# Kernel optimization log

Hardware: AMD Instinct MI355X
Metric: run time of the kernel (lower is better)

Reference implementation:

```python
import jax, jax.numpy as jnp
import numpy as np

N_I = 500_000   # 'indivi' nodes (dst)
N_H = 200_000   # 'house' nodes
F_I = 32        # indivi feature dim
F_H = 16        # house feature dim
EF = 8          # edge_attr dim
E1 = 2_000_000  # house->indivi edges
E2 = 2_000_000  # indivi->indivi edges


def setup_inputs() -> dict:
    key = jax.random.key(0)
    ks = jax.random.split(key, 16)
    return {
        "x_indivi": jax.random.normal(ks[0], (N_I, F_I), jnp.float32),
        "x_house": jax.random.normal(ks[1], (N_H, F_H), jnp.float32),
        "edge_attr_h2i": jax.random.normal(ks[2], (E1, EF), jnp.float32),
        "edge_attr_i2i": jax.random.normal(ks[3], (E2, EF), jnp.float32),
        "W_edge_h2i": jax.random.normal(ks[4], (F_H, EF), jnp.float32) * 0.1,
        "b_edge_h2i": jax.random.normal(ks[5], (F_H,), jnp.float32) * 0.1,
        "W_edge_i2i": jax.random.normal(ks[6], (F_I, EF), jnp.float32) * 0.1,
        "b_edge_i2i": jax.random.normal(ks[7], (F_I,), jnp.float32) * 0.1,
        "W_root_h2i": jax.random.normal(ks[8], (1, F_I), jnp.float32) * 0.1,
        "bias_h2i": jax.random.normal(ks[9], (1,), jnp.float32) * 0.1,
        "W_root_i2i": jax.random.normal(ks[10], (1, F_I), jnp.float32) * 0.1,
        "bias_i2i": jax.random.normal(ks[11], (1,), jnp.float32) * 0.1,
        "src_h2i": jax.random.randint(ks[12], (E1,), 0, N_H, jnp.int32),
        "dst_h2i": jax.random.randint(ks[13], (E1,), 0, N_I, jnp.int32),
        "src_i2i": jax.random.randint(ks[14], (E2,), 0, N_I, jnp.int32),
        "dst_i2i": jax.random.randint(ks[15], (E2,), 0, N_I, jnp.int32),
    }


def _nnconv(x_src, x_dst, edge_attr, src, dst, W_edge, b_edge, W_root, bias, num_dst):
    # Edge MLP -> per-edge weight matrix of shape [F_src, out=1], flattened to [E, F_src]
    w = edge_attr @ W_edge.T + b_edge                     # [E, F_src]
    # message_e = x_src[src_e] @ w_e  (out_channels = 1)
    msg = jnp.sum(x_src[src] * w, axis=-1, keepdims=True)  # [E, 1]
    agg = jax.ops.segment_sum(msg, dst, num_segments=num_dst)  # [N_dst, 1]
    # root transform on destination features + bias
    return agg + x_dst @ W_root.T + bias                  # [N_dst, 1]


def reference(x_indivi, x_house, edge_attr_h2i, edge_attr_i2i,
              W_edge_h2i, b_edge_h2i, W_edge_i2i, b_edge_i2i,
              W_root_h2i, bias_h2i, W_root_i2i, bias_i2i,
              src_h2i, dst_h2i, src_i2i, dst_i2i):
    out_h = _nnconv(x_house, x_indivi, edge_attr_h2i, src_h2i, dst_h2i,
                    W_edge_h2i, b_edge_h2i, W_root_h2i, bias_h2i, N_I)
    out_i = _nnconv(x_indivi, x_indivi, edge_attr_i2i, src_i2i, dst_i2i,
                    W_edge_i2i, b_edge_i2i, W_root_i2i, bias_i2i, N_I)
    # HeteroConv(aggr='sum') over the two relations targeting 'indivi'
    return out_h + out_i
```

## Files before the change

kernel.cpp:

```cpp
#include <hip/hip_runtime.h>

#define N_I 500000
#define N_H 200000
#define E1  2000000
#define E2  2000000
#define TOTAL_E (E1 + E2)

#define BSHIFT 12
#define NB 128
#define NBK ((N_I + 4095) / 4096)
#define CHUNK 2048
#define NWG ((TOTAL_E + CHUNK - 1) / CHUNK)
#define WPT 8

template<int F, bool ROOT>
__global__ __launch_bounds__(256) void precompute_g(
    const float* __restrict__ x, const float* __restrict__ W, const float* __restrict__ b,
    float* __restrict__ g, int n,
    const float* __restrict__ rW1, const float* __restrict__ rW2,
    const float* __restrict__ rb1, const float* __restrict__ rb2,
    float* __restrict__ out)
{
    __shared__ float Wf[F * 8];
    __shared__ float bv[F];
    __shared__ float wr[F];

    for (int i = threadIdx.x; i < F * 8; i += 256) Wf[i] = W[i];
    if (threadIdx.x < F) {
        bv[threadIdx.x] = b[threadIdx.x];
        if (ROOT) wr[threadIdx.x] = rW1[threadIdx.x] + rW2[threadIdx.x];
    }
    __syncthreads();

    int nid = blockIdx.x * 256 + threadIdx.x;
    if (nid >= n) return;

    float xv[F];
    const float4* xp = (const float4*)(x + (size_t)nid * F);
    #pragma unroll
    for (int q = 0; q < F / 4; q++) {
        float4 v = xp[q];
        xv[q*4+0] = v.x; xv[q*4+1] = v.y; xv[q*4+2] = v.z; xv[q*4+3] = v.w;
    }

    float acc[9];
    #pragma unroll
    for (int k = 0; k < 9; k++) acc[k] = 0.f;

    #pragma unroll
    for (int j = 0; j < F; j++) {
        float4 w0 = *(const float4*)(Wf + j * 8);
        float4 w1 = *(const float4*)(Wf + j * 8 + 4);
        float xj = xv[j];
        acc[0] = fmaf(xj, w0.x, acc[0]);
        acc[1] = fmaf(xj, w0.y, acc[1]);
        acc[2] = fmaf(xj, w0.z, acc[2]);
        acc[3] = fmaf(xj, w0.w, acc[3]);
        acc[4] = fmaf(xj, w1.x, acc[4]);
        acc[5] = fmaf(xj, w1.y, acc[5]);
        acc[6] = fmaf(xj, w1.z, acc[6]);
        acc[7] = fmaf(xj, w1.w, acc[7]);
        acc[8] = fmaf(xj, bv[j], acc[8]);
    }

    float4* gp = (float4*)(g + (size_t)nid * 12);
    gp[0] = make_float4(acc[0], acc[1], acc[2], acc[3]);
    gp[1] = make_float4(acc[4], acc[5], acc[6], acc[7]);
    gp[2] = make_float4(acc[8], 0.f, 0.f, 0.f);

    if (ROOT) {
        float r = rb1[0] + rb2[0];
        #pragma unroll
        for (int j = 0; j < F; j++) r = fmaf(xv[j], wr[j], r);
        out[nid] = r;
    }
}

__device__ __forceinline__ void edge_msg(
    int t,
    const int* __restrict__ src1, const int* __restrict__ dst1,
    const float* __restrict__ ea1, const float* __restrict__ g1,
    const int* __restrict__ src2, const int* __restrict__ dst2,
    const float* __restrict__ ea2, const float* __restrict__ g2,
    int& d_out, float& m_out)
{
    const int* srcp; const int* dstp; const float* eap; const float* gp;
    int e;
    if (t < E1) { e = t;      srcp = src1; dstp = dst1; eap = ea1; gp = g1; }
    else        { e = t - E1; srcp = src2; dstp = dst2; eap = ea2; gp = g2; }

    int s = srcp[e];
    d_out = dstp[e];
    const float4* ap = (const float4*)(eap + (size_t)e * 8);
    float4 a0 = ap[0];
    float4 a1 = ap[1];
    const float4* gr = (const float4*)(gp + (size_t)s * 12);
    float4 ga = gr[0];
    float4 gb = gr[1];
    float4 gc = gr[2];

    float msg = gc.x;
    msg = fmaf(a0.x, ga.x, msg);
    msg = fmaf(a0.y, ga.y, msg);
    msg = fmaf(a0.z, ga.z, msg);
    msg = fmaf(a0.w, ga.w, msg);
    msg = fmaf(a1.x, gb.x, msg);
    msg = fmaf(a1.y, gb.y, msg);
    msg = fmaf(a1.z, gb.z, msg);
    msg = fmaf(a1.w, gb.w, msg);
    m_out = msg;
}

__global__ __launch_bounds__(256) void msg_hist_kernel(
    const int* __restrict__ src1, const int* __restrict__ dst1,
    const float* __restrict__ ea1, const float* __restrict__ g1,
    const int* __restrict__ src2, const int* __restrict__ dst2,
    const float* __restrict__ ea2, const float* __restrict__ g2,
    float* __restrict__ msg_out, int* __restrict__ H)
{
    __shared__ int hist[NB];
    if (threadIdx.x < NB) hist[threadIdx.x] = 0;
    __syncthreads();

    int base = blockIdx.x * CHUNK;
    #pragma unroll
    for (int it = 0; it < CHUNK / 256; ++it) {
        int t = base + it * 256 + threadIdx.x;
        if (t < TOTAL_E) {
            int d; float m;
            edge_msg(t, src1, dst1, ea1, g1, src2, dst2, ea2, g2, d, m);
            msg_out[t] = m;
            atomicAdd(&hist[d >> BSHIFT], 1);
        }
    }
    __syncthreads();
    if (threadIdx.x < NB) H[blockIdx.x * NB + threadIdx.x] = hist[threadIdx.x];
}

__global__ __launch_bounds__(256) void scan_cols_kernel(int* __restrict__ H,
                                                        int* __restrict__ total)
{
    __shared__ int sums[256];
    int b = blockIdx.x;
    int tid = threadIdx.x;

    int vals[WPT];
    int s = 0;
    #pragma unroll
    for (int k = 0; k < WPT; k++) {
        int w = tid * WPT + k;
        vals[k] = (w < NWG) ? H[w * NB + b] : 0;
        s += vals[k];
    }
    sums[tid] = s;
    __syncthreads();
    for (int off = 1; off < 256; off <<= 1) {
        int t = (tid >= off) ? sums[tid - off] : 0;
        __syncthreads();
        sums[tid] += t;
        __syncthreads();
    }
    int run = sums[tid] - s;
    #pragma unroll
    for (int k = 0; k < WPT; k++) {
        int w = tid * WPT + k;
        if (w < NWG) H[w * NB + b] = run;
        run += vals[k];
    }
    if (tid == 255) total[b] = sums[255];
}

__global__ __launch_bounds__(128) void scan_base_kernel(const int* __restrict__ total,
                                                        int* __restrict__ base)
{
    __shared__ int v[NB];
    int tid = threadIdx.x;
    int orig = total[tid];
    v[tid] = orig;
    __syncthreads();
    for (int off = 1; off < NB; off <<= 1) {
        int t = (tid >= off) ? v[tid - off] : 0;
        __syncthreads();
        v[tid] += t;
        __syncthreads();
    }
    base[tid] = v[tid] - orig;
}

__global__ __launch_bounds__(256) void scatter_kernel(
    const int* __restrict__ dst1, const int* __restrict__ dst2,
    const float* __restrict__ msg, const int* __restrict__ H,
    const int* __restrict__ base, uint2* __restrict__ pairs)
{
    __shared__ int cnt[NB];
    __shared__ int sv[NB];
    __shared__ int gbase[NB];
    __shared__ unsigned short bkt[CHUNK];
    __shared__ uint2 lp[CHUNK];

    int tid = threadIdx.x;
    if (tid < NB) cnt[tid] = 0;
    __syncthreads();

    int cbase = blockIdx.x * CHUNK;
    int dloc[CHUNK / 256];
    #pragma unroll
    for (int it = 0; it < CHUNK / 256; ++it) {
        int t = cbase + it * 256 + tid;
        int d = -1;
        if (t < TOTAL_E) {
            d = (t < E1) ? dst1[t] : dst2[t - E1];
            atomicAdd(&cnt[d >> BSHIFT], 1);
        }
        dloc[it] = d;
    }
    __syncthreads();

    int myc = 0;
    if (tid < NB) { myc = cnt[tid]; sv[tid] = myc; }
    __syncthreads();
    for (int off = 1; off < NB; off <<= 1) {
        int t = (tid < NB && tid >= off) ? sv[tid - off] : 0;
        __syncthreads();
        if (tid < NB) sv[tid] += t;
        __syncthreads();
    }
    if (tid < NB) {
        int loff = sv[tid] - myc;
        gbase[tid] = H[blockIdx.x * NB + tid] + base[tid] - loff;
        cnt[tid] = loff;
    }
    __syncthreads();

    #pragma unroll
    for (int it = 0; it < CHUNK / 256; ++it) {
        int t = cbase + it * 256 + tid;
        if (t < TOTAL_E) {
            int d = dloc[it];
            float m = msg[t];
            int b = d >> BSHIFT;
            int slot = atomicAdd(&cnt[b], 1);
            lp[slot] = make_uint2((unsigned)d, __float_as_uint(m));
            bkt[slot] = (unsigned short)b;
        }
    }
    __syncthreads();

    int nvalid = TOTAL_E - cbase;
    if (nvalid > CHUNK) nvalid = CHUNK;
    for (int i = tid; i < nvalid; i += 256) {
        int b = bkt[i];
        pairs[gbase[b] + i] = lp[i];
    }
}

__global__ __launch_bounds__(512) void reduce_kernel(
    const uint2* __restrict__ pairs, const int* __restrict__ base,
    const int* __restrict__ total, float* __restrict__ part)
{
    __shared__ float acc[4096];
    for (int i = threadIdx.x; i < 4096; i += 512) acc[i] = 0.f;
    __syncthreads();

    int b = blockIdx.x >> 2;
    int k = blockIdx.x & 3;
    int start = base[b];
    int cnt = total[b];
    int q = (cnt + 3) >> 2;
    int s0 = k * q;
    int s1 = s0 + q; if (s1 > cnt) s1 = cnt;

    for (int i = s0 + threadIdx.x; i < s1; i += 512) {
        uint2 p = pairs[start + i];
        atomicAdd(&acc[p.x & 4095], __uint_as_float(p.y));
    }
    __syncthreads();

    float* dp = part + (size_t)blockIdx.x * 4096;
    for (int i = threadIdx.x; i < 4096; i += 512) dp[i] = acc[i];
}

__global__ __launch_bounds__(256) void merge_kernel(
    const float* __restrict__ part, float* __restrict__ out)
{
    int n = blockIdx.x * 256 + threadIdx.x;
    if (n < N_I) {
        int b = n >> BSHIFT;
        int i = n & 4095;
        const float* p = part + (size_t)b * 4 * 4096 + i;
        out[n] += (p[0] + p[4096]) + (p[8192] + p[12288]);
    }
}

__global__ __launch_bounds__(256) void edge_kernel_atomic(
    const int* __restrict__ src1, const int* __restrict__ dst1,
    const float* __restrict__ ea1, const float* __restrict__ g1,
    const int* __restrict__ src2, const int* __restrict__ dst2,
    const float* __restrict__ ea2, const float* __restrict__ g2,
    float* __restrict__ out)
{
    int t = blockIdx.x * 256 + threadIdx.x;
    if (t >= TOTAL_E) return;
    int d; float m;
    edge_msg(t, src1, dst1, ea1, g1, src2, dst2, ea2, g2, d, m);
    atomicAdd(out + d, m);
}

extern "C" void kernel_launch(void* const* d_in, const int* in_sizes, int n_in,
                              void* d_out, int out_size, void* d_ws, size_t ws_size,
                              hipStream_t stream) {
    const float* x_i  = (const float*)d_in[0];
    const float* x_h  = (const float*)d_in[1];
    const float* ea_h = (const float*)d_in[2];
    const float* ea_i = (const float*)d_in[3];
    const float* We_h = (const float*)d_in[4];
    const float* be_h = (const float*)d_in[5];
    const float* We_i = (const float*)d_in[6];
    const float* be_i = (const float*)d_in[7];
    const float* Wr_h = (const float*)d_in[8];
    const float* br_h = (const float*)d_in[9];
    const float* Wr_i = (const float*)d_in[10];
    const float* br_i = (const float*)d_in[11];
    const int* src_h = (const int*)d_in[12];
    const int* dst_h = (const int*)d_in[13];
    const int* src_i = (const int*)d_in[14];
    const int* dst_i = (const int*)d_in[15];

    float* out = (float*)d_out;

    char* ws = (char*)d_ws;
    float* g_i   = (float*)ws;
    float* g_h   = (float*)(ws + 24000000);
    uint2* pairs = (uint2*)ws;
    float* msg   = (float*)(ws + 33600000);
    float* part  = (float*)(ws + 33600000);
    int*   H     = (int*)  (ws + 49600000);
    int*   tot   = (int*)  (ws + 50600448);
    int*   bas   = (int*)  (ws + 50602496);
    const size_t WS_NEEDED = 50603008;

    precompute_g<16, false><<<(N_H + 255) / 256, 256, 0, stream>>>(
        x_h, We_h, be_h, g_h, N_H, nullptr, nullptr, nullptr, nullptr, nullptr);
    precompute_g<32, true><<<(N_I + 255) / 256, 256, 0, stream>>>(
        x_i, We_i, be_i, g_i, N_I, Wr_h, Wr_i, br_h, br_i, out);

    if (ws_size >= WS_NEEDED) {
        msg_hist_kernel<<<NWG, 256, 0, stream>>>(
            src_h, dst_h, ea_h, g_h, src_i, dst_i, ea_i, g_i, msg, H);
        scan_cols_kernel<<<NB, 256, 0, stream>>>(H, tot);
        scan_base_kernel<<<1, NB, 0, stream>>>(tot, bas);
        scatter_kernel<<<NWG, 256, 0, stream>>>(
            dst_h, dst_i, msg, H, bas, pairs);
        reduce_kernel<<<NBK * 4, 512, 0, stream>>>(pairs, bas, tot, part);
        merge_kernel<<<(N_I + 255) / 256, 256, 0, stream>>>(part, out);
    } else {
        edge_kernel_atomic<<<(TOTAL_E + 255) / 256, 256, 0, stream>>>(
            src_h, dst_h, ea_h, g_h, src_i, dst_i, ea_i, g_i, out);
    }
}
```

Before: 368.2 us.

## Fuse message computation into scatter and compact g and pair layouts

The histogram pass now reads only destination indices. Message computation moves into the scatter kernel, which drops the intermediate msg array write and re-read. The per-node g table is split into an 8-float vector plus a separate scalar, replacing the padded 12-float row. Sorted pairs become a float message plus a 16-bit local index instead of 8-byte pairs, which cuts scatter and reduce traffic. Edge loads are batched four at a time to raise memory-level parallelism, at the cost of more registers in the scatter kernel.

```diff
diff --git a/kernel.cpp b/kernel.cpp
--- a/kernel.cpp
+++ b/kernel.cpp
@@ -12,11 +12,12 @@
 #define CHUNK 2048
 #define NWG ((TOTAL_E + CHUNK - 1) / CHUNK)
 #define WPT 8
+#define ITERS (CHUNK / 256)
 
 template<int F, bool ROOT>
 __global__ __launch_bounds__(256) void precompute_g(
     const float* __restrict__ x, const float* __restrict__ W, const float* __restrict__ b,
-    float* __restrict__ g, int n,
+    float* __restrict__ g8, float* __restrict__ gc, int n,
     const float* __restrict__ rW1, const float* __restrict__ rW2,
     const float* __restrict__ rb1, const float* __restrict__ rb2,
     float* __restrict__ out)
@@ -63,10 +64,10 @@
         acc[8] = fmaf(xj, bv[j], acc[8]);
     }
 
-    float4* gp = (float4*)(g + (size_t)nid * 12);
+    float4* gp = (float4*)(g8 + (size_t)nid * 8);
     gp[0] = make_float4(acc[0], acc[1], acc[2], acc[3]);
     gp[1] = make_float4(acc[4], acc[5], acc[6], acc[7]);
-    gp[2] = make_float4(acc[8], 0.f, 0.f, 0.f);
+    gc[nid] = acc[8];
 
     if (ROOT) {
         float r = rb1[0] + rb2[0];
@@ -76,47 +77,9 @@
     }
 }
 
-__device__ __forceinline__ void edge_msg(
-    int t,
-    const int* __restrict__ src1, const int* __restrict__ dst1,
-    const float* __restrict__ ea1, const float* __restrict__ g1,
-    const int* __restrict__ src2, const int* __restrict__ dst2,
-    const float* __restrict__ ea2, const float* __restrict__ g2,
-    int& d_out, float& m_out)
-{
-    const int* srcp; const int* dstp; const float* eap; const float* gp;
-    int e;
-    if (t < E1) { e = t;      srcp = src1; dstp = dst1; eap = ea1; gp = g1; }
-    else        { e = t - E1; srcp = src2; dstp = dst2; eap = ea2; gp = g2; }
-
-    int s = srcp[e];
-    d_out = dstp[e];
-    const float4* ap = (const float4*)(eap + (size_t)e * 8);
-    float4 a0 = ap[0];
-    float4 a1 = ap[1];
-    const float4* gr = (const float4*)(gp + (size_t)s * 12);
-    float4 ga = gr[0];
-    float4 gb = gr[1];
-    float4 gc = gr[2];
-
-    float msg = gc.x;
-    msg = fmaf(a0.x, ga.x, msg);
-    msg = fmaf(a0.y, ga.y, msg);
-    msg = fmaf(a0.z, ga.z, msg);
-    msg = fmaf(a0.w, ga.w, msg);
-    msg = fmaf(a1.x, gb.x, msg);
-    msg = fmaf(a1.y, gb.y, msg);
-    msg = fmaf(a1.z, gb.z, msg);
-    msg = fmaf(a1.w, gb.w, msg);
-    m_out = msg;
-}
-
-__global__ __launch_bounds__(256) void msg_hist_kernel(
-    const int* __restrict__ src1, const int* __restrict__ dst1,
-    const float* __restrict__ ea1, const float* __restrict__ g1,
-    const int* __restrict__ src2, const int* __restrict__ dst2,
-    const float* __restrict__ ea2, const float* __restrict__ g2,
-    float* __restrict__ msg_out, int* __restrict__ H)
+__global__ __launch_bounds__(256) void hist_kernel(
+    const int* __restrict__ dst1, const int* __restrict__ dst2,
+    int* __restrict__ H)
 {
     __shared__ int hist[NB];
     if (threadIdx.x < NB) hist[threadIdx.x] = 0;
@@ -124,12 +87,10 @@
 
     int base = blockIdx.x * CHUNK;
     #pragma unroll
-    for (int it = 0; it < CHUNK / 256; ++it) {
+    for (int it = 0; it < ITERS; ++it) {
         int t = base + it * 256 + threadIdx.x;
         if (t < TOTAL_E) {
-            int d; float m;
-            edge_msg(t, src1, dst1, ea1, g1, src2, dst2, ea2, g2, d, m);
-            msg_out[t] = m;
+            int d = (t < E1) ? dst1[t] : dst2[t - E1];
             atomicAdd(&hist[d >> BSHIFT], 1);
         }
     }
@@ -187,33 +148,112 @@
     base[tid] = v[tid] - orig;
 }
 
-__global__ __launch_bounds__(256) void scatter_kernel(
-    const int* __restrict__ dst1, const int* __restrict__ dst2,
-    const float* __restrict__ msg, const int* __restrict__ H,
-    const int* __restrict__ base, uint2* __restrict__ pairs)
+__device__ __forceinline__ void compute_msgs8(
+    int tid, int ebase,
+    const int* __restrict__ src, const int* __restrict__ dst,
+    const float* __restrict__ ea, const float4* __restrict__ g8,
+    const float* __restrict__ gc,
+    int* dloc, float* mloc)
+{
+    int sl[ITERS];
+    #pragma unroll
+    for (int it = 0; it < ITERS; ++it) {
+        int e = ebase + it * 256 + tid;
+        sl[it] = src[e];
+        dloc[it] = dst[e];
+    }
+    #pragma unroll
+    for (int h = 0; h < 2; ++h) {
+        float4 ga[4], gb[4], a0[4], a1[4];
+        float gv[4];
+        #pragma unroll
+        for (int k = 0; k < 4; ++k) {
+            int it = h * 4 + k;
+            int e = ebase + it * 256 + tid;
+            int s = sl[it];
+            ga[k] = g8[(size_t)s * 2];
+            gb[k] = g8[(size_t)s * 2 + 1];
+            gv[k] = gc[s];
+            const float4* ap = (const float4*)(ea + (size_t)e * 8);
+            a0[k] = ap[0];
+            a1[k] = ap[1];
+        }
+        #pragma unroll
+        for (int k = 0; k < 4; ++k) {
+            float m = gv[k];
+            m = fmaf(a0[k].x, ga[k].x, m);
+            m = fmaf(a0[k].y, ga[k].y, m);
+            m = fmaf(a0[k].z, ga[k].z, m);
+            m = fmaf(a0[k].w, ga[k].w, m);
+            m = fmaf(a1[k].x, gb[k].x, m);
+            m = fmaf(a1[k].y, gb[k].y, m);
+            m = fmaf(a1[k].z, gb[k].z, m);
+            m = fmaf(a1[k].w, gb[k].w, m);
+            mloc[h * 4 + k] = m;
+        }
+    }
+}
+
+__global__ __launch_bounds__(256) void scatter_fused_kernel(
+    const int* __restrict__ src1, const int* __restrict__ dst1,
+    const float* __restrict__ ea1, const float4* __restrict__ g8_1, const float* __restrict__ gc_1,
+    const int* __restrict__ src2, const int* __restrict__ dst2,
+    const float* __restrict__ ea2, const float4* __restrict__ g8_2, const float* __restrict__ gc_2,
+    const int* __restrict__ H, const int* __restrict__ base,
+    float* __restrict__ msgs_out, unsigned short* __restrict__ lidx_out)
 {
     __shared__ int cnt[NB];
     __shared__ int sv[NB];
     __shared__ int gbase[NB];
-    __shared__ unsigned short bkt[CHUNK];
-    __shared__ uint2 lp[CHUNK];
+    __shared__ unsigned int lu[CHUNK];
+    __shared__ float lm[CHUNK];
 
     int tid = threadIdx.x;
     if (tid < NB) cnt[tid] = 0;
     __syncthreads();
 
     int cbase = blockIdx.x * CHUNK;
-    int dloc[CHUNK / 256];
-    #pragma unroll
-    for (int it = 0; it < CHUNK / 256; ++it) {
-        int t = cbase + it * 256 + tid;
-        int d = -1;
-        if (t < TOTAL_E) {
-            d = (t < E1) ? dst1[t] : dst2[t - E1];
-            atomicAdd(&cnt[d >> BSHIFT], 1);
+    int dloc[ITERS];
+    float mloc[ITERS];
+
+    if (cbase + CHUNK <= E1) {
+        compute_msgs8(tid, cbase, src1, dst1, ea1, g8_1, gc_1, dloc, mloc);
+    } else if (cbase >= E1 && cbase + CHUNK <= TOTAL_E) {
+        compute_msgs8(tid, cbase - E1, src2, dst2, ea2, g8_2, gc_2, dloc, mloc);
+    } else {
+        #pragma unroll
+        for (int it = 0; it < ITERS; ++it) {
+            int t = cbase + it * 256 + tid;
+            int d = -1; float m = 0.f;
+            if (t < TOTAL_E) {
+                const int* srcp; const int* dstp; const float* eap;
+                const float4* g8p; const float* gcp; int e;
+                if (t < E1) { e = t;      srcp = src1; dstp = dst1; eap = ea1; g8p = g8_1; gcp = gc_1; }
+                else        { e = t - E1; srcp = src2; dstp = dst2; eap = ea2; g8p = g8_2; gcp = gc_2; }
+                int s = srcp[e];
+                d = dstp[e];
+                float4 ga = g8p[(size_t)s * 2];
+                float4 gb = g8p[(size_t)s * 2 + 1];
+                const float4* ap = (const float4*)(eap + (size_t)e * 8);
+                float4 a0 = ap[0];
+                float4 a1 = ap[1];
+                m = gcp[s];
+                m = fmaf(a0.x, ga.x, m);
+                m = fmaf(a0.y, ga.y, m);
+                m = fmaf(a0.z, ga.z, m);
+                m = fmaf(a0.w, ga.w, m);
+                m = fmaf(a1.x, gb.x, m);
+                m = fmaf(a1.y, gb.y, m);
+                m = fmaf(a1.z, gb.z, m);
+                m = fmaf(a1.w, gb.w, m);
+            }
+            dloc[it] = d; mloc[it] = m;
         }
-        dloc[it] = d;
-    }
+    }
+
+    #pragma unroll
+    for (int it = 0; it < ITERS; ++it)
+        if (dloc[it] >= 0) atomicAdd(&cnt[dloc[it] >> BSHIFT], 1);
     __syncthreads();
 
     int myc = 0;
@@ -233,15 +273,13 @@
     __syncthreads();
 
     #pragma unroll
-    for (int it = 0; it < CHUNK / 256; ++it) {
-        int t = cbase + it * 256 + tid;
-        if (t < TOTAL_E) {
-            int d = dloc[it];
-            float m = msg[t];
+    for (int it = 0; it < ITERS; ++it) {
+        int d = dloc[it];
+        if (d >= 0) {
             int b = d >> BSHIFT;
             int slot = atomicAdd(&cnt[b], 1);
-            lp[slot] = make_uint2((unsigned)d, __float_as_uint(m));
-            bkt[slot] = (unsigned short)b;
+            lu[slot] = ((unsigned)b << BSHIFT) | (unsigned)(d & 4095);
+            lm[slot] = mloc[it];
         }
     }
     __syncthreads();
@@ -249,14 +287,18 @@
     int nvalid = TOTAL_E - cbase;
     if (nvalid > CHUNK) nvalid = CHUNK;
     for (int i = tid; i < nvalid; i += 256) {
-        int b = bkt[i];
-        pairs[gbase[b] + i] = lp[i];
+        unsigned u = lu[i];
+        int b = (int)(u >> BSHIFT);
+        int g = gbase[b] + i;
+        msgs_out[g] = lm[i];
+        lidx_out[g] = (unsigned short)(u & 4095u);
     }
 }
 
 __global__ __launch_bounds__(512) void reduce_kernel(
-    const uint2* __restrict__ pairs, const int* __restrict__ base,
-    const int* __restrict__ total, float* __restrict__ part)
+    const float* __restrict__ msgs, const unsigned short* __restrict__ lidx,
+    const int* __restrict__ base, const int* __restrict__ total,
+    float* __restrict__ part)
 {
     __shared__ float acc[4096];
     for (int i = threadIdx.x; i < 4096; i += 512) acc[i] = 0.f;
@@ -271,8 +313,7 @@
     int s1 = s0 + q; if (s1 > cnt) s1 = cnt;
 
     for (int i = s0 + threadIdx.x; i < s1; i += 512) {
-        uint2 p = pairs[start + i];
-        atomicAdd(&acc[p.x & 4095], __uint_as_float(p.y));
+        atomicAdd(&acc[lidx[start + i]], msgs[start + i]);
     }
     __syncthreads();
 
@@ -294,15 +335,33 @@
 
 __global__ __launch_bounds__(256) void edge_kernel_atomic(
     const int* __restrict__ src1, const int* __restrict__ dst1,
-    const float* __restrict__ ea1, const float* __restrict__ g1,
+    const float* __restrict__ ea1, const float4* __restrict__ g8_1, const float* __restrict__ gc_1,
     const int* __restrict__ src2, const int* __restrict__ dst2,
-    const float* __restrict__ ea2, const float* __restrict__ g2,
+    const float* __restrict__ ea2, const float4* __restrict__ g8_2, const float* __restrict__ gc_2,
     float* __restrict__ out)
 {
     int t = blockIdx.x * 256 + threadIdx.x;
     if (t >= TOTAL_E) return;
-    int d; float m;
-    edge_msg(t, src1, dst1, ea1, g1, src2, dst2, ea2, g2, d, m);
+    const int* srcp; const int* dstp; const float* eap;
+    const float4* g8p; const float* gcp; int e;
+    if (t < E1) { e = t;      srcp = src1; dstp = dst1; eap = ea1; g8p = g8_1; gcp = gc_1; }
+    else        { e = t - E1; srcp = src2; dstp = dst2; eap = ea2; g8p = g8_2; gcp = gc_2; }
+    int s = srcp[e];
+    int d = dstp[e];
+    float4 ga = g8p[(size_t)s * 2];
+    float4 gb = g8p[(size_t)s * 2 + 1];
+    const float4* ap = (const float4*)(eap + (size_t)e * 8);
+    float4 a0 = ap[0];
+    float4 a1 = ap[1];
+    float m = gcp[s];
+    m = fmaf(a0.x, ga.x, m);
+    m = fmaf(a0.y, ga.y, m);
+    m = fmaf(a0.z, ga.z, m);
+    m = fmaf(a0.w, ga.w, m);
+    m = fmaf(a1.x, gb.x, m);
+    m = fmaf(a1.y, gb.y, m);
+    m = fmaf(a1.z, gb.z, m);
+    m = fmaf(a1.w, gb.w, m);
     atomicAdd(out + d, m);
 }
 
@@ -329,32 +388,36 @@
     float* out = (float*)d_out;
 
     char* ws = (char*)d_ws;
-    float* g_i   = (float*)ws;
-    float* g_h   = (float*)(ws + 24000000);
-    uint2* pairs = (uint2*)ws;
-    float* msg   = (float*)(ws + 33600000);
-    float* part  = (float*)(ws + 33600000);
-    int*   H     = (int*)  (ws + 49600000);
-    int*   tot   = (int*)  (ws + 50600448);
-    int*   bas   = (int*)  (ws + 50602496);
-    const size_t WS_NEEDED = 50603008;
+    float* g8_i = (float*)ws;
+    float* g8_h = (float*)(ws + 16000000);
+    float* gc_i = (float*)(ws + 22400000);
+    float* gc_h = (float*)(ws + 24400000);
+    float* msgs = (float*)(ws + 25200000);
+    unsigned short* lidx = (unsigned short*)(ws + 41200000);
+    float* part = (float*)ws;
+    int*   H    = (int*)(ws + 49200000);
+    int*   tot  = (int*)(ws + 50200448);
+    int*   bas  = (int*)(ws + 50201472);
+    const size_t WS_NEEDED = 50201984;
 
     precompute_g<16, false><<<(N_H + 255) / 256, 256, 0, stream>>>(
-        x_h, We_h, be_h, g_h, N_H, nullptr, nullptr, nullptr, nullptr, nullptr);
+        x_h, We_h, be_h, g8_h, gc_h, N_H, nullptr, nullptr, nullptr, nullptr, nullptr);
     precompute_g<32, true><<<(N_I + 255) / 256, 256, 0, stream>>>(
-        x_i, We_i, be_i, g_i, N_I, Wr_h, Wr_i, br_h, br_i, out);
+        x_i, We_i, be_i, g8_i, gc_i, N_I, Wr_h, Wr_i, br_h, br_i, out);
 
     if (ws_size >= WS_NEEDED) {
-        msg_hist_kernel<<<NWG, 256, 0, stream>>>(
-            src_h, dst_h, ea_h, g_h, src_i, dst_i, ea_i, g_i, msg, H);
+        hist_kernel<<<NWG, 256, 0, stream>>>(dst_h, dst_i, H);
         scan_cols_kernel<<<NB, 256, 0, stream>>>(H, tot);
         scan_base_kernel<<<1, NB, 0, stream>>>(tot, bas);
-        scatter_kernel<<<NWG, 256, 0, stream>>>(
-            dst_h, dst_i, msg, H, bas, pairs);
-        reduce_kernel<<<NBK * 4, 512, 0, stream>>>(pairs, bas, tot, part);
+        scatter_fused_kernel<<<NWG, 256, 0, stream>>>(
+            src_h, dst_h, ea_h, (const float4*)g8_h, gc_h,
+            src_i, dst_i, ea_i, (const float4*)g8_i, gc_i,
+            H, bas, msgs, lidx);
+        reduce_kernel<<<NBK * 4, 512, 0, stream>>>(msgs, lidx, bas, tot, part);
         merge_kernel<<<(N_I + 255) / 256, 256, 0, stream>>>(part, out);
     } else {
         edge_kernel_atomic<<<(TOTAL_E + 255) / 256, 256, 0, stream>>>(
-            src_h, dst_h, ea_h, g_h, src_i, dst_i, ea_i, g_i, out);
-    }
-}
+            src_h, dst_h, ea_h, (const float4*)g8_h, gc_h,
+            src_i, dst_i, ea_i, (const float4*)g8_i, gc_i, out);
+    }
+}
```

New measurement: 372.4 us. Within noise of the previous version (+1.1%).
